# Optimization experiments

Measured on AMD Instinct MI355X. Metric: run time of the kernel, lower is better.

The kernel has to match this reference:

```python
import jax, jax.numpy as jnp
import numpy as np

B, L, C, PS, K, NL, NH, DFF, MAXLEN = 64, 4096, 32, 16, 1024, 4, 8, 2048, 512
D = PS * C          # code_dim = 512
P = L // PS         # num_patches = 256
PA_H = 4            # heads in PatchCrossAttention (largest of {4,2,1} dividing C)
COMMIT = 0.25


def _ln(x, g, b, eps=1e-5):
    m = x.mean(-1, keepdims=True)
    v = x.var(-1, keepdims=True)
    return (x - m) / jnp.sqrt(v + eps) * g + b


def _mha(q, k, v, w_in, b_in, w_out, b_out, nh, mask=None):
    # torch nn.MultiheadAttention math: in_proj weight [3d, d], y = x @ W.T + b
    d = q.shape[-1]
    dh = d // nh
    wq, wk, wv = jnp.split(w_in, 3, axis=0)
    bq, bk, bv = jnp.split(b_in, 3, axis=0)
    qh = (q @ wq.T + bq).reshape(q.shape[0], q.shape[1], nh, dh)
    kh = (k @ wk.T + bk).reshape(k.shape[0], k.shape[1], nh, dh)
    vh = (v @ wv.T + bv).reshape(v.shape[0], v.shape[1], nh, dh)
    scores = jnp.einsum('bqhd,bkhd->bhqk', qh, kh) / jnp.sqrt(jnp.asarray(dh, q.dtype))
    if mask is not None:
        scores = jnp.where(mask, jnp.asarray(-jnp.inf, scores.dtype), scores)
    a = jax.nn.softmax(scores, axis=-1)
    o = jnp.einsum('bhqk,bkhd->bqhd', a, vh).reshape(q.shape[0], q.shape[1], d)
    return o @ w_out.T + b_out


def _forward(x, pa_lq, pa_pos, pa_win, pa_bin, pa_wout, pa_bout,
             pa_ln1g, pa_ln1b, pa_ln2g, pa_ln2b, pa_w1, pa_b1, pa_w2, pa_b2,
             cb, tf_pos, tf_win, tf_bin, tf_wout, tf_bout,
             tf_ln1g, tf_ln1b, tf_ln2g, tf_ln2b,
             tf_w1, tf_b1, tf_w2, tf_b2, fin_g, fin_b):
    Bx = x.shape[0]
    # --- patchify: [B, L, C] -> [B*P, PS, C] ---
    xp = x.reshape(Bx * P, PS, C)
    # --- PatchCrossAttention ---
    x_pos = xp + pa_pos                       # pos emb over patch steps
    lq = jnp.broadcast_to(pa_lq, xp.shape)    # learnable query tokens
    attn = _mha(lq, x_pos, x_pos, pa_win, pa_bin, pa_wout, pa_bout, PA_H)
    xn = _ln(lq + attn, pa_ln1g, pa_ln1b)
    f = jax.nn.gelu(xn @ pa_w1 + pa_b1, approximate=False) @ pa_w2 + pa_b2
    xo = _ln(xn + f, pa_ln2g, pa_ln2b)
    enc = xp + xo                             # residual to raw patch
    # --- flatten + VQ ---
    z = enc.reshape(Bx * P, D)
    d2 = (z * z).sum(1, keepdims=True) + (cb * cb).sum(1) - 2.0 * (z @ cb.T)
    idx = jnp.argmin(d2, axis=1)
    q = cb[idx]
    sg = jax.lax.stop_gradient
    e_loss = jnp.mean((sg(q) - z) ** 2)
    q_loss = jnp.mean((q - sg(z)) ** 2)
    vq_loss = q_loss + COMMIT * e_loss
    quant = z + sg(q - z)                     # straight-through
    # --- causal transformer over code sequence [B, P, D] ---
    t = quant.reshape(Bx, P, D) + tf_pos[:P]
    causal = jnp.triu(jnp.ones((P, P), dtype=bool), 1)
    for i in range(NL):  # post-LN TransformerEncoderLayer, gelu
        a = _mha(t, t, t, tf_win[i], tf_bin[i], tf_wout[i], tf_bout[i], NH, causal)
        t = _ln(t + a, tf_ln1g[i], tf_ln1b[i])
        f = jax.nn.gelu(t @ tf_w1[i] + tf_b1[i], approximate=False) @ tf_w2[i] + tf_b2[i]
        t = _ln(t + f, tf_ln2g[i], tf_ln2b[i])
    y = _ln(t, fin_g, fin_b)
    return y, vq_loss, idx


def setup_inputs() -> dict:
    key = jax.random.key(0)
    ks = iter(jax.random.split(key, 32))
    n = lambda shape, s=0.02: jax.random.normal(next(ks), shape, dtype=jnp.float32) * s
    inp = {
        'x': jax.random.normal(next(ks), (B, L, C), dtype=jnp.float32),
        'pa_lq': n((PS, C)), 'pa_pos': n((PS, C)),
        'pa_win': n((3 * C, C)), 'pa_bin': jnp.zeros((3 * C,), jnp.float32),
        'pa_wout': n((C, C)), 'pa_bout': jnp.zeros((C,), jnp.float32),
        'pa_ln1g': jnp.ones((C,), jnp.float32), 'pa_ln1b': jnp.zeros((C,), jnp.float32),
        'pa_ln2g': jnp.ones((C,), jnp.float32), 'pa_ln2b': jnp.zeros((C,), jnp.float32),
        'pa_w1': n((C, 2 * C)), 'pa_b1': jnp.zeros((2 * C,), jnp.float32),
        'pa_w2': n((2 * C, C)), 'pa_b2': jnp.zeros((C,), jnp.float32),
        'cb': jax.random.uniform(next(ks), (K, D), jnp.float32, -1.0 / K, 1.0 / K),
        'tf_pos': n((MAXLEN, D)),
        'tf_win': n((NL, 3 * D, D)), 'tf_bin': jnp.zeros((NL, 3 * D), jnp.float32),
        'tf_wout': n((NL, D, D)), 'tf_bout': jnp.zeros((NL, D), jnp.float32),
        'tf_ln1g': jnp.ones((NL, D), jnp.float32), 'tf_ln1b': jnp.zeros((NL, D), jnp.float32),
        'tf_ln2g': jnp.ones((NL, D), jnp.float32), 'tf_ln2b': jnp.zeros((NL, D), jnp.float32),
        'tf_w1': n((NL, D, DFF)), 'tf_b1': jnp.zeros((NL, DFF), jnp.float32),
        'tf_w2': n((NL, DFF, D)), 'tf_b2': jnp.zeros((NL, D), jnp.float32),
        'fin_g': jnp.ones((D,), jnp.float32), 'fin_b': jnp.zeros((D,), jnp.float32),
    }
    return inp


def reference(x, pa_lq, pa_pos, pa_win, pa_bin, pa_wout, pa_bout,
              pa_ln1g, pa_ln1b, pa_ln2g, pa_ln2b, pa_w1, pa_b1, pa_w2, pa_b2,
              cb, tf_pos, tf_win, tf_bin, tf_wout, tf_bout,
              tf_ln1g, tf_ln1b, tf_ln2g, tf_ln2b,
              tf_w1, tf_b1, tf_w2, tf_b2, fin_g, fin_b):
    return _forward(x, pa_lq, pa_pos, pa_win, pa_bin, pa_wout, pa_bout,
                    pa_ln1g, pa_ln1b, pa_ln2g, pa_ln2b, pa_w1, pa_b1, pa_w2, pa_b2,
                    cb, tf_pos, tf_win, tf_bin, tf_wout, tf_bout,
                    tf_ln1g, tf_ln1b, tf_ln2g, tf_ln2b,
                    tf_w1, tf_b1, tf_w2, tf_b2, fin_g, fin_b)
```

## Files before the change

kernel.cpp:

```cpp
#include <hip/hip_runtime.h>


#define SQRT1_2F 0.70710678118654752440f

typedef __attribute__((ext_vector_type(8))) short short8;
typedef __attribute__((ext_vector_type(4))) float f32x4;
typedef __attribute__((ext_vector_type(8))) unsigned short ushort8;
typedef unsigned short ushort;
typedef unsigned long long u64;

__device__ __forceinline__ float gelu_exact(float v) {
  return 0.5f * v * (1.0f + erff(v * SQRT1_2F));
}

__device__ __forceinline__ ushort f2b_rne(float f) {
  unsigned u = __float_as_uint(f);
  unsigned r = (u + 0x7fffu + ((u >> 16) & 1u)) >> 16;
  return (ushort)r;
}

__device__ __forceinline__ float b2f(ushort u) {
  return __uint_as_float(((unsigned)u) << 16);
}

__device__ __forceinline__ void gload16(const void* g, void* l) {
  __builtin_amdgcn_global_load_lds(
      (const __attribute__((address_space(1))) void*)g,
      (__attribute__((address_space(3))) void*)l, 16, 0, 0);
}

__device__ __forceinline__ unsigned fkey(float d) {
  unsigned u = __float_as_uint(d);
  return (u & 0x80000000u) ? ~u : (u | 0x80000000u);
}

__global__ __launch_bounds__(64) void patch_setup_kernel(
    const float* __restrict__ lq, const float* __restrict__ win,
    const float* __restrict__ bin, const float* __restrict__ w1,
    const float* __restrict__ w2, float* __restrict__ q16,
    float* __restrict__ w1T, float* __restrict__ w2T) {
  const int tid = threadIdx.x;
#pragma unroll
  for (int q = 0; q < 8; q++) {
    int e = tid + (q << 6);
    int i = e >> 5, c = e & 31;
    const float* wr = win + (size_t)c * 32;
    float acc = bin[c];
#pragma unroll
    for (int d = 0; d < 32; d++) acc += lq[(i << 5) + d] * wr[d];
    q16[e] = acc;
  }
#pragma unroll
  for (int q = 0; q < 32; q++) {
    int e = tid + (q << 6);
    int u = e >> 5, d = e & 31;
    w1T[e] = w1[(size_t)d * 64 + u];
  }
#pragma unroll
  for (int q = 0; q < 32; q++) {
    int e = tid + (q << 6);
    int c = e >> 6, u = e & 63;
    w2T[e] = w2[(size_t)u * 32 + c];
  }
}

__device__ __forceinline__ void ln_16xS(float* buf, const float* g,
                                        const float* bb, int tid) {
  int row = tid >> 2, sub = tid & 3;
  int c0 = sub << 3;
  float* r = buf + row * 34 + c0;
  float v[8];
  float s = 0.f, s2 = 0.f;
#pragma unroll
  for (int n = 0; n < 8; n++) {
    float t = r[n];
    v[n] = t; s += t; s2 += t * t;
  }
  s += __shfl_xor(s, 1);  s += __shfl_xor(s, 2);
  s2 += __shfl_xor(s2, 1); s2 += __shfl_xor(s2, 2);
  float m = s * (1.0f / 32.0f);
  float var = s2 * (1.0f / 32.0f) - m * m;
  float inv = 1.0f / sqrtf(var + 1e-5f);
#pragma unroll
  for (int n = 0; n < 8; n++)
    r[n] = (v[n] - m) * inv * g[c0 + n] + bb[c0 + n];
}

__global__ __launch_bounds__(256) void pkA_kernel(
    const float* __restrict__ x, const float* __restrict__ pos,
    const float* __restrict__ win, const float* __restrict__ bin,
    const float* __restrict__ q16, float* __restrict__ so) {
  __shared__ float sxp[2048];
  __shared__ float skv[4096];
  __shared__ float sq16[16 * 33];
  const int blk = blockIdx.x, t = threadIdx.x;
  const int p0 = blk << 2;
  const int cfix = t & 31;

#pragma unroll
  for (int q = 0; q < 8; q++) {
    int e = t + (q << 8);
    int pl = e >> 9, r = e & 511;
    sxp[e] = x[(size_t)(p0 + pl) * 512 + r] + pos[r];
  }
  if (t < 128) {
#pragma unroll
    for (int q = 0; q < 4; q++) {
      int e = t + (q << 7);
      sq16[(e >> 5) * 33 + (e & 31)] = q16[e];
    }
  }

  float wr0[32], wr1[32];
#pragma unroll
  for (int d4 = 0; d4 < 8; d4++) {
    *(float4*)(wr0 + 4 * d4) =
        *(const float4*)(win + (size_t)(32 + cfix) * 32 + 4 * d4);
    *(float4*)(wr1 + 4 * d4) =
        *(const float4*)(win + (size_t)(64 + cfix) * 32 + 4 * d4);
  }
  const float bk = bin[32 + cfix];
  const float bv = bin[64 + cfix];
  __syncthreads();

#pragma unroll
  for (int q = 0; q < 16; q++) {
    int e = t + (q << 8);
    int pl = e >> 10, rr = e & 1023;
    int w = rr >> 9, rj = rr & 511, j = rj >> 5;
    const float* sx = sxp + (pl << 9) + (j << 5);
    const float* wreg = w ? wr1 : wr0;
    float acc = w ? bv : bk;
#pragma unroll
    for (int d = 0; d < 32; d++) acc += sx[d] * wreg[d];
    skv[e] = acc;
  }
  __syncthreads();

  const int pl = t >> 6, hh = (t >> 4) & 3, i = t & 15;
  const int p = p0 + pl;
  const float* kp = skv + (pl << 10);
  const int hd = hh << 3;

  float sc[16];
#pragma unroll
  for (int j = 0; j < 16; j++) {
    float acc = 0.f;
#pragma unroll
    for (int d = 0; d < 8; d++)
      acc += sq16[i * 33 + hd + d] * kp[(j << 5) + hd + d];
    sc[j] = acc * 0.35355339059327373f;
  }
  {
    float mx = sc[0];
#pragma unroll
    for (int j = 1; j < 16; j++) mx = fmaxf(mx, sc[j]);
    float sm = 0.f;
    float ev[16];
#pragma unroll
    for (int j = 0; j < 16; j++) { ev[j] = expf(sc[j] - mx); sm += ev[j]; }
    float inv = 1.0f / sm;
#pragma unroll
    for (int j = 0; j < 16; j++) sc[j] = ev[j] * inv;
  }
  float* orow = so + (size_t)p * 512 + (i << 5) + hd;
#pragma unroll
  for (int c8 = 0; c8 < 8; c8++) {
    const int c = hd + c8;
    float acc = 0.f;
#pragma unroll
    for (int j = 0; j < 16; j++) acc += sc[j] * kp[512 + (j << 5) + c];
    orow[c8] = acc;
  }
}

__global__ __launch_bounds__(64) void pkB_kernel(
    const float* __restrict__ so_g, const float* __restrict__ x,
    const float* __restrict__ wout, const float* __restrict__ bout,
    const float* __restrict__ lq,
    const float* __restrict__ ln1g, const float* __restrict__ ln1b,
    const float* __restrict__ w1T, const float* __restrict__ b1,
    const float* __restrict__ w2T, const float* __restrict__ b2,
    const float* __restrict__ ln2g, const float* __restrict__ ln2b,
    float* __restrict__ z, ushort* __restrict__ zh,
    ushort* __restrict__ zl, float* __restrict__ znorm) {
  __shared__ float sso[544], sst[544], ssh[1056];
  const int p = blockIdx.x, t = threadIdx.x;
  const int cfix = t & 31;

#pragma unroll
  for (int q = 0; q < 8; q++) {
    int e = t + (q << 6);
    sso[(e >> 5) * 34 + (e & 31)] = so_g[(size_t)p * 512 + e];
  }

  float wo[32];
#pragma unroll
  for (int d4 = 0; d4 < 8; d4++)
    *(float4*)(wo + 4 * d4) = *(const float4*)(wout + (size_t)cfix * 32 + 4 * d4);
  __syncthreads();

#pragma unroll
  for (int q = 0; q < 8; q++) {
    int e = t + (q << 6);
    int i = e >> 5;
    float acc = bout[cfix];
#pragma unroll
    for (int d = 0; d < 32; d++) acc += sso[i * 34 + d] * wo[d];
    sst[i * 34 + cfix] = acc + lq[(i << 5) + cfix];
  }
  __syncthreads();
  ln_16xS(sst, ln1g, ln1b, t);

  float w1r[32];
#pragma unroll
  for (int d4 = 0; d4 < 8; d4++)
    *(float4*)(w1r + 4 * d4) = *(const float4*)(w1T + (size_t)t * 32 + 4 * d4);
  __syncthreads();

#pragma unroll
  for (int q = 0; q < 16; q++) {
    int i = q;
    float acc = b1[t];
#pragma unroll
    for (int d = 0; d < 32; d++) acc += sst[i * 34 + d] * w1r[d];
    ssh[i * 66 + t] = gelu_exact(acc);
  }

  float w2r[64];
#pragma unroll
  for (int u4 = 0; u4 < 16; u4++)
    *(float4*)(w2r + 4 * u4) = *(const float4*)(w2T + (size_t)cfix * 64 + 4 * u4);
  __syncthreads();

#pragma unroll
  for (int q = 0; q < 8; q++) {
    int e = t + (q << 6);
    int i = e >> 5;
    float acc = b2[cfix];
#pragma unroll
    for (int u = 0; u < 64; u++) acc += ssh[i * 66 + u] * w2r[u];
    sso[i * 34 + cfix] = acc + sst[i * 34 + cfix];
  }
  __syncthreads();
  ln_16xS(sso, ln2g, ln2b, t);
  __syncthreads();

  const float* xp = x + (size_t)p * 512;
  const int row = t >> 2, c0v = (t & 3) << 3;
  float zv[8];
#pragma unroll
  for (int n = 0; n < 8; n++)
    zv[n] = xp[(t << 3) + n] + sso[row * 34 + c0v + n];
  float* zo = z + (size_t)p * 512 + (t << 3);
  *(float4*)(zo)     = *(float4*)(zv);
  *(float4*)(zo + 4) = *(float4*)(zv + 4);
  ushort8 hv, lv;
  float s2 = 0.f;
#pragma unroll
  for (int n = 0; n < 8; n++) {
    s2 += zv[n] * zv[n];
    ushort h = f2b_rne(zv[n]);
    hv[n] = h;
    lv[n] = f2b_rne(zv[n] - b2f(h));
  }
  *(ushort8*)(zh + (size_t)p * 512 + (t << 3)) = hv;
  *(ushort8*)(zl + (size_t)p * 512 + (t << 3)) = lv;
#pragma unroll
  for (int off = 1; off < 64; off <<= 1) s2 += __shfl_xor(s2, off);
  if (t == 0) znorm[p] = s2;
}

__global__ __launch_bounds__(64) void cbnorm_kernel(
    const float* __restrict__ cb, float* __restrict__ cbn,
    ushort* __restrict__ ch, ushort* __restrict__ cl) {
  int c = blockIdx.x, lane = threadIdx.x;
  const float* r = cb + (size_t)c * 512 + lane * 8;
  float v[8];
  *(float4*)(v)     = *(const float4*)(r);
  *(float4*)(v + 4) = *(const float4*)(r + 4);
  float s = 0.f;
  ushort8 hv, lv;
#pragma unroll
  for (int n = 0; n < 8; n++) {
    s += v[n] * v[n];
    ushort h = f2b_rne(v[n]);
    hv[n] = h;
    lv[n] = f2b_rne(v[n] - b2f(h));
  }
  *(ushort8*)(ch + (size_t)c * 512 + lane * 8) = hv;
  *(ushort8*)(cl + (size_t)c * 512 + lane * 8) = lv;
#pragma unroll
  for (int off = 1; off < 64; off <<= 1) s += __shfl_xor(s, off);
  if (lane == 0) cbn[c] = s;
}

__global__ __launch_bounds__(256) void gemm_vq_b3(
    const ushort* __restrict__ Ah, const ushort* __restrict__ Al,
    const ushort* __restrict__ Bh, const ushort* __restrict__ Bl,
    const float* __restrict__ znorm, const float* __restrict__ cbn,
    u64* __restrict__ packed) {
  __shared__ ushort sAh[4096], sAl[4096], sBh[4096], sBl[4096];
  const int cpx = gridDim.x >> 3;
  const int bid = (blockIdx.x & 7) * cpx + (blockIdx.x >> 3);
  const int bx = bid & 7, by = bid >> 3;
  const int m0 = by << 7, n0 = bx << 7;
  const int tid = threadIdx.x;
  const int wid = tid >> 6, lane = tid & 63;
  const int wr = wid >> 1, wc = wid & 1;
  const int l15 = lane & 15, lk = lane >> 4;

  const f32x4 fzero = {0.f, 0.f, 0.f, 0.f};
  f32x4 acc[4][4];
#pragma unroll
  for (int i = 0; i < 4; i++)
#pragma unroll
    for (int j = 0; j < 4; j++) acc[i][j] = fzero;

  for (int k0 = 0; k0 < 512; k0 += 32) {
#pragma unroll
    for (int c = 0; c < 2; c++) {
      const int I = tid + (c << 8);
      const int r = I >> 2, kk = (I & 3) << 3;
      const size_t ga = (size_t)(m0 + r) * 512 + k0 + kk;
      const size_t gb = (size_t)(n0 + r) * 512 + k0 + kk;
      const size_t lo = (size_t)((wid << 6) + (c << 8)) * 8;
      gload16(Ah + ga, sAh + lo);
      gload16(Al + ga, sAl + lo);
      gload16(Bh + gb, sBh + lo);
      gload16(Bl + gb, sBl + lo);
    }
    __syncthreads();

    short8 ah[4], al[4], bh[4], bl[4];
#pragma unroll
    for (int m = 0; m < 4; m++) {
      const int ar = ((wr << 6) + (m << 4) + l15) * 32 + lk * 8;
      ah[m] = *(const short8*)(sAh + ar);
      al[m] = *(const short8*)(sAl + ar);
      const int br = ((wc << 6) + (m << 4) + l15) * 32 + lk * 8;
      bh[m] = *(const short8*)(sBh + br);
      bl[m] = *(const short8*)(sBl + br);
    }
#pragma unroll
    for (int m = 0; m < 4; m++)
#pragma unroll
      for (int n = 0; n < 4; n++) {
        acc[m][n] = __builtin_amdgcn_mfma_f32_16x16x32_bf16(ah[m], bh[n],
                                                            acc[m][n], 0, 0, 0);
        acc[m][n] = __builtin_amdgcn_mfma_f32_16x16x32_bf16(ah[m], bl[n],
                                                            acc[m][n], 0, 0, 0);
        acc[m][n] = __builtin_amdgcn_mfma_f32_16x16x32_bf16(al[m], bh[n],
                                                            acc[m][n], 0, 0, 0);
      }
    __syncthreads();
  }

  float zn[4][4];
#pragma unroll
  for (int m = 0; m < 4; m++)
#pragma unroll
    for (int r = 0; r < 4; r++)
      zn[m][r] = znorm[m0 + (wr << 6) + (m << 4) + (lk << 2) + r];
  float cbnv[4];
#pragma unroll
  for (int n = 0; n < 4; n++)
    cbnv[n] = cbn[n0 + (wc << 6) + (n << 4) + l15];

#pragma unroll
  for (int m = 0; m < 4; m++) {
#pragma unroll
    for (int r = 0; r < 4; r++) {
      u64 best = ~0ull;
#pragma unroll
      for (int n = 0; n < 4; n++) {
        const int gcol = n0 + (wc << 6) + (n << 4) + l15;
        float d = (zn[m][r] + cbnv[n]) - 2.0f * acc[m][n][r];
        u64 key = ((u64)fkey(d) << 32) | (unsigned)gcol;
        best = best < key ? best : key;
      }
#pragma unroll
      for (int off = 1; off < 16; off <<= 1) {
        u64 o = __shfl_xor(best, off);
        best = best < o ? best : o;
      }
      if (l15 == 0) {
        const int grow = m0 + (wr << 6) + (m << 4) + (lk << 2) + r;
        atomicMin(&packed[grow], best);
      }
    }
  }
}

__global__ __launch_bounds__(256) void vq_slim_kernel(
    const u64* __restrict__ packed, const float* __restrict__ cb,
    const float* __restrict__ z, const float* __restrict__ tf_pos,
    float* __restrict__ t, ushort* __restrict__ th,
    float* __restrict__ idx_out, float* __restrict__ loss_part) {
  __shared__ float spart[4];
  const int wv = threadIdx.x >> 6;
  const int r = (blockIdx.x << 2) + wv;
  const int lane = threadIdx.x & 63;
  const int bi = (int)(unsigned)(packed[r] & 0xFFFFFFFFull);
  const float* zr = z + (size_t)r * 512 + (lane << 3);
  const float* q = cb + (size_t)bi * 512 + (lane << 3);
  const float* pr = tf_pos + (size_t)(r & 255) * 512 + (lane << 3);
  float zv[8], qv[8], pv[8];
  *(float4*)(zv)     = *(const float4*)(zr);
  *(float4*)(zv + 4) = *(const float4*)(zr + 4);
  *(float4*)(qv)     = *(const float4*)(q);
  *(float4*)(qv + 4) = *(const float4*)(q + 4);
  *(float4*)(pv)     = *(const float4*)(pr);
  *(float4*)(pv + 4) = *(const float4*)(pr + 4);
  float lsum = 0.f;
  float tv[8];
  ushort8 w;
#pragma unroll
  for (int n = 0; n < 8; n++) {
    float diff = qv[n] - zv[n];
    lsum += diff * diff;
    tv[n] = qv[n] + pv[n];
    w[n] = f2b_rne(tv[n]);
  }
  float* to = t + (size_t)r * 512 + (lane << 3);
  *(float4*)(to)     = *(float4*)(tv);
  *(float4*)(to + 4) = *(float4*)(tv + 4);
  *(ushort8*)(th + (size_t)r * 512 + (lane << 3)) = w;
#pragma unroll
  for (int off = 1; off < 64; off <<= 1) lsum += __shfl_xor(lsum, off);
  if (lane == 0) {
    idx_out[r] = (float)bi;
    spart[wv] = lsum;
  }
  __syncthreads();
  if (threadIdx.x == 0)
    loss_part[blockIdx.x] = (spart[0] + spart[1]) + (spart[2] + spart[3]);
}

__global__ __launch_bounds__(256) void loss_reduce_kernel(
    const float* __restrict__ loss_part, float* __restrict__ loss_out) {
  __shared__ float sw[4];
  float s = 0.f;
  for (int i = threadIdx.x; i < 4096; i += 256) s += loss_part[i];
#pragma unroll
  for (int off = 1; off < 64; off <<= 1) s += __shfl_xor(s, off);
  const int wv = threadIdx.x >> 6;
  if ((threadIdx.x & 63) == 0) sw[wv] = s;
  __syncthreads();
  if (threadIdx.x == 0)
    loss_out[0] = ((sw[0] + sw[1]) + (sw[2] + sw[3])) * (1.25f / 8388608.0f);
}

template <int OUTMODE>
__global__ __launch_bounds__(256) void gemm_bf16_kernel(
    const ushort* __restrict__ A, const ushort* __restrict__ B,
    const float* __restrict__ bias, void* __restrict__ Cout,
    int M, int N, int K) {
  __shared__ ushort As[4096];
  __shared__ ushort Bs[4096];
  const int nbx = N >> 7;
  const int cpx = gridDim.x >> 3;
  const int bid = (blockIdx.x & 7) * cpx + (blockIdx.x >> 3);
  const int bx = bid % nbx, by = bid / nbx;
  const int m0 = by << 7, n0 = bx << 7;
  const int tid = threadIdx.x;
  const int wid = tid >> 6, lane = tid & 63;
  const int wr = wid >> 1, wc = wid & 1;
  const int l15 = lane & 15, lk = lane >> 4;

  const f32x4 fzero = {0.f, 0.f, 0.f, 0.f};
  f32x4 acc[4][4];
#pragma unroll
  for (int i = 0; i < 4; i++)
#pragma unroll
    for (int j = 0; j < 4; j++) acc[i][j] = fzero;

  for (int k0 = 0; k0 < K; k0 += 32) {
#pragma unroll
    for (int c = 0; c < 2; c++) {
      const int I = tid + (c << 8);
      const int r = I >> 2, kk = (I & 3) << 3;
      gload16(A + (size_t)(m0 + r) * K + k0 + kk,
              As + (size_t)((wid << 6) + (c << 8)) * 8);
      gload16(B + (size_t)(n0 + r) * K + k0 + kk,
              Bs + (size_t)((wid << 6) + (c << 8)) * 8);
    }
    __syncthreads();

    short8 a[4], b[4];
#pragma unroll
    for (int m = 0; m < 4; m++) {
      const int ar = (wr << 6) + (m << 4) + l15;
      a[m] = *(const short8*)(As + ar * 32 + lk * 8);
      const int br = (wc << 6) + (m << 4) + l15;
      b[m] = *(const short8*)(Bs + br * 32 + lk * 8);
    }
#pragma unroll
    for (int m = 0; m < 4; m++)
#pragma unroll
      for (int n = 0; n < 4; n++)
        acc[m][n] = __builtin_amdgcn_mfma_f32_16x16x32_bf16(a[m], b[n],
                                                            acc[m][n], 0, 0, 0);
    __syncthreads();
  }

  float bv[4];
#pragma unroll
  for (int n = 0; n < 4; n++)
    bv[n] = bias[n0 + (wc << 6) + (n << 4) + l15];

#pragma unroll
  for (int m = 0; m < 4; m++) {
#pragma unroll
    for (int n = 0; n < 4; n++) {
      const int gcol = n0 + (wc << 6) + (n << 4) + l15;
#pragma unroll
      for (int r = 0; r < 4; r++) {
        const int grow = m0 + (wr << 6) + (m << 4) + (lk << 2) + r;
        float v = acc[m][n][r] + bv[n];
        if (OUTMODE == 0) {
          ((float*)Cout)[(size_t)grow * N + gcol] = v;
        } else if (OUTMODE == 1) {
          ((ushort*)Cout)[(size_t)grow * N + gcol] = f2b_rne(gelu_exact(v));
        } else {
          ((ushort*)Cout)[(size_t)grow * N + gcol] = f2b_rne(v);
        }
      }
    }
  }
}

__global__ void cvt_flat(const float* __restrict__ in, ushort* __restrict__ out,
                         int n) {
  int i = blockIdx.x * blockDim.x + threadIdx.x;
  const int stride = gridDim.x * blockDim.x;
  for (; i < n; i += stride) out[i] = f2b_rne(in[i]);
}

__global__ __launch_bounds__(256) void cvt_tr(const float* __restrict__ in,
                                              ushort* __restrict__ out,
                                              int R, int C) {
  __shared__ float tile[32][33];
  const int bc = blockIdx.x, br = blockIdx.y, lay = blockIdx.z;
  const float* src = in + (size_t)lay * R * C;
  ushort* dst = out + (size_t)lay * R * C;
  const int tid = threadIdx.x;
#pragma unroll
  for (int q = 0; q < 4; q++) {
    int idx = tid + (q << 8);
    int rr = idx >> 5, cc = idx & 31;
    tile[rr][cc] = src[(size_t)(br * 32 + rr) * C + bc * 32 + cc];
  }
  __syncthreads();
#pragma unroll
  for (int q = 0; q < 4; q++) {
    int idx = tid + (q << 8);
    int co = idx >> 5, ro = idx & 31;
    dst[(size_t)(bc * 32 + co) * R + br * 32 + ro] = f2b_rne(tile[ro][co]);
  }
}

__global__ __launch_bounds__(64) void attn_mfma_kernel(
    const ushort* __restrict__ qkv, ushort* __restrict__ o) {
  __shared__ ushort lds[8192];
  char* KsB = (char*)lds;
  char* VtB = (char*)(lds + 4096);
  const int bid = blockIdx.x;
  const int xcd = bid & 7, slot = bid >> 3;
  const int b = (xcd << 3) | (slot >> 5);
  const int h = (slot >> 2) & 7;
  const int qb = slot & 3;
  const int lane = threadIdx.x;
  const int l15 = lane & 15, lk4 = lane >> 4;

  short8 qf[4][2];
#pragma unroll
  for (int m = 0; m < 4; m++)
#pragma unroll
    for (int kc = 0; kc < 2; kc++)
      qf[m][kc] = *(const short8*)(qkv +
          (size_t)(b * 256 + qb * 64 + m * 16 + l15) * 1536 +
          h * 64 + kc * 32 + lk4 * 8);

  const f32x4 fz = {0.f, 0.f, 0.f, 0.f};
  f32x4 O[4][4];
#pragma unroll
  for (int m = 0; m < 4; m++)
#pragma unroll
    for (int n = 0; n < 4; n++) O[m][n] = fz;
  float lsum[4][4];
#pragma unroll
  for (int m = 0; m < 4; m++)
#pragma unroll
    for (int r = 0; r < 4; r++) lsum[m][r] = 0.f;

  for (int jt = 0; jt <= qb; jt++) {
    ushort8 kv[8], vv[8];
    const ushort* krow = qkv + (size_t)(b * 256 + jt * 64 + lane) * 1536 +
                         512 + h * 64;
#pragma unroll
    for (int u = 0; u < 8; u++) kv[u] = ((const ushort8*)krow)[u];
#pragma unroll
    for (int u = 0; u < 8; u++) vv[u] = ((const ushort8*)(krow + 512))[u];
    __syncthreads();
    {
      const int rx = (lane & 7) << 4;
#pragma unroll
      for (int u = 0; u < 8; u++)
        *(ushort8*)(KsB + lane * 128 + ((u << 4) ^ rx)) = kv[u];
#pragma unroll
      for (int u = 0; u < 8; u++)
#pragma unroll
        for (int i = 0; i < 8; i++) {
          const int d = u * 8 + i;
          *(ushort*)(VtB + ((d * 128 + lane * 2) ^ ((d & 7) << 4))) =
              (ushort)vv[u][i];
        }
    }
    __syncthreads();

    f32x4 sacc[4][4];
#pragma unroll
    for (int m = 0; m < 4; m++)
#pragma unroll
      for (int n = 0; n < 4; n++) sacc[m][n] = fz;
#pragma unroll
    for (int kc = 0; kc < 2; kc++) {
      short8 bf[4];
#pragma unroll
      for (int n = 0; n < 4; n++) {
        const int row = n * 16 + l15;
        bf[n] = *(const short8*)(KsB + row * 128 +
                                 ((kc * 64 + lk4 * 16) ^ ((row & 7) << 4)));
      }
#pragma unroll
      for (int m = 0; m < 4; m++)
#pragma unroll
        for (int n = 0; n < 4; n++)
          sacc[m][n] = __builtin_amdgcn_mfma_f32_16x16x32_bf16(
              qf[m][kc], bf[n], sacc[m][n], 0, 0, 0);
    }
    __syncthreads();

    const bool diag = (jt == qb);
#pragma unroll
    for (int m = 0; m < 4; m++)
#pragma unroll
      for (int n = 0; n < 4; n++)
#pragma unroll
        for (int r = 0; r < 4; r++) {
          const int ql = m * 16 + lk4 * 4 + r;
          const int jl = n * 16 + l15;
          float e = __expf(sacc[m][n][r] * 0.125f);
          if (diag && jl > ql) e = 0.f;
          const ushort pu = f2b_rne(e);
          lsum[m][r] += b2f(pu);
          *(ushort*)(KsB + ql * 128 + ((jl * 2) ^ ((ql & 7) << 4))) = pu;
        }
    __syncthreads();

#pragma unroll
    for (int kc = 0; kc < 2; kc++) {
      short8 pf[4], vf[4];
#pragma unroll
      for (int m = 0; m < 4; m++) {
        const int row = m * 16 + l15;
        pf[m] = *(const short8*)(KsB + row * 128 +
                                 ((kc * 64 + lk4 * 16) ^ ((row & 7) << 4)));
      }
#pragma unroll
      for (int n = 0; n < 4; n++) {
        const int row = n * 16 + l15;
        vf[n] = *(const short8*)(VtB + row * 128 +
                                 ((kc * 64 + lk4 * 16) ^ ((row & 7) << 4)));
      }
#pragma unroll
      for (int m = 0; m < 4; m++)
#pragma unroll
        for (int n = 0; n < 4; n++)
          O[m][n] = __builtin_amdgcn_mfma_f32_16x16x32_bf16(
              pf[m], vf[n], O[m][n], 0, 0, 0);
    }
  }

  float inv[4][4];
#pragma unroll
  for (int m = 0; m < 4; m++)
#pragma unroll
    for (int r = 0; r < 4; r++) {
      float v = lsum[m][r];
      v += __shfl_xor(v, 1); v += __shfl_xor(v, 2);
      v += __shfl_xor(v, 4); v += __shfl_xor(v, 8);
      inv[m][r] = 1.0f / v;
    }
#pragma unroll
  for (int m = 0; m < 4; m++)
#pragma unroll
    for (int n = 0; n < 4; n++)
#pragma unroll
      for (int r = 0; r < 4; r++) {
        const int row = b * 256 + qb * 64 + m * 16 + lk4 * 4 + r;
        const int col = h * 64 + n * 16 + l15;
        o[(size_t)row * 512 + col] = f2b_rne(O[m][n][r] * inv[m][r]);
      }
}

__global__ __launch_bounds__(256) void ln_kernel(
    const float* __restrict__ xin, const float* __restrict__ addin,
    const float* __restrict__ g, const float* __restrict__ bb,
    float* __restrict__ outp, ushort* __restrict__ outb) {
  const int r = blockIdx.x * 4 + (threadIdx.x >> 6);
  const int lane = threadIdx.x & 63;
  const float* xr = xin + (size_t)r * 512 + lane * 8;
  float v[8];
  *(float4*)(v)     = *(const float4*)(xr);
  *(float4*)(v + 4) = *(const float4*)(xr + 4);
  if (addin) {
    const float* ar = addin + (size_t)r * 512 + lane * 8;
    float w[8];
    *(float4*)(w)     = *(const float4*)(ar);
    *(float4*)(w + 4) = *(const float4*)(ar + 4);
#pragma unroll
    for (int n = 0; n < 8; n++) v[n] += w[n];
  }
  float s = 0.f, s2 = 0.f;
#pragma unroll
  for (int n = 0; n < 8; n++) { s += v[n]; s2 += v[n] * v[n]; }
#pragma unroll
  for (int off = 1; off < 64; off <<= 1) {
    s += __shfl_xor(s, off);
    s2 += __shfl_xor(s2, off);
  }
  float m = s * (1.0f / 512.0f);
  float var = s2 * (1.0f / 512.0f) - m * m;
  float inv = 1.0f / sqrtf(var + 1e-5f);
  const int c0 = lane * 8;
  float outv[8];
#pragma unroll
  for (int n = 0; n < 8; n++) outv[n] = (v[n] - m) * inv * g[c0 + n] + bb[c0 + n];
  float* orow = outp + (size_t)r * 512 + c0;
  *(float4*)(orow)     = *(float4*)(outv);
  *(float4*)(orow + 4) = *(float4*)(outv + 4);
  if (outb) {
    ushort8 w;
#pragma unroll
    for (int n = 0; n < 8; n++) w[n] = f2b_rne(outv[n]);
    *(ushort8*)(outb + (size_t)r * 512 + c0) = w;
  }
}

extern "C" void kernel_launch(void* const* d_in, const int* in_sizes, int n_in,
                              void* d_out, int out_size, void* d_ws, size_t ws_size,
                              hipStream_t stream) {
  const float* x       = (const float*)d_in[0];
  const float* pa_lq   = (const float*)d_in[1];
  const float* pa_pos  = (const float*)d_in[2];
  const float* pa_win  = (const float*)d_in[3];
  const float* pa_bin  = (const float*)d_in[4];
  const float* pa_wout = (const float*)d_in[5];
  const float* pa_bout = (const float*)d_in[6];
  const float* pa_ln1g = (const float*)d_in[7];
  const float* pa_ln1b = (const float*)d_in[8];
  const float* pa_ln2g = (const float*)d_in[9];
  const float* pa_ln2b = (const float*)d_in[10];
  const float* pa_w1   = (const float*)d_in[11];
  const float* pa_b1   = (const float*)d_in[12];
  const float* pa_w2   = (const float*)d_in[13];
  const float* pa_b2   = (const float*)d_in[14];
  const float* cb      = (const float*)d_in[15];
  const float* tf_pos  = (const float*)d_in[16];
  const float* tf_win  = (const float*)d_in[17];
  const float* tf_bin  = (const float*)d_in[18];
  const float* tf_wout = (const float*)d_in[19];
  const float* tf_bout = (const float*)d_in[20];
  const float* tf_ln1g = (const float*)d_in[21];
  const float* tf_ln1b = (const float*)d_in[22];
  const float* tf_ln2g = (const float*)d_in[23];
  const float* tf_ln2b = (const float*)d_in[24];
  const float* tf_w1   = (const float*)d_in[25];
  const float* tf_b1   = (const float*)d_in[26];
  const float* tf_w2   = (const float*)d_in[27];
  const float* tf_b2   = (const float*)d_in[28];
  const float* fin_g   = (const float*)d_in[29];
  const float* fin_b   = (const float*)d_in[30];

  float* yout = (float*)d_out;
  float* loss_out = yout + 8388608;
  float* idx_out = loss_out + 1;

  float* ws   = (float*)d_ws;
  float* z    = ws;
  float* tb   = z + 8388608;
  float* bufA = tb + 8388608;
  float* bufC = bufA + 16777216;
  float* wreg = bufC + 8388608;
  float* treg = wreg + 6291456;
  float* cbn  = treg + 4194304;
  float* q16  = cbn + 1024;
  float* w1T  = q16 + 512;
  float* w2T  = w1T + 2048;
  float* znorm = w2T + 2048;
  u64*   packed = (u64*)(znorm + 16384);
  float* loss_part = (float*)(packed + 16384);

  ushort* win_b  = (ushort*)wreg;
  ushort* wout_b = win_b + 3145728;
  ushort* w1t_b  = wout_b + 1048576;
  ushort* w2t_b  = w1t_b + 4194304;
  ushort* tbh    = (ushort*)treg;
  ushort* qkvh   = (ushort*)bufA;
  ushort* abh    = (ushort*)z;
  ushort* zh_b   = (ushort*)bufC;
  ushort* zl_b   = zh_b + 8388608;
  ushort* ch_b   = (ushort*)treg;
  ushort* cl_b   = ch_b + 524288;

  hipMemsetAsync(packed, 0xFF, 16384 * sizeof(u64), stream);
  cbnorm_kernel<<<1024, 64, 0, stream>>>(cb, cbn, ch_b, cl_b);
  patch_setup_kernel<<<1, 64, 0, stream>>>(pa_lq, pa_win, pa_bin, pa_w1,
                                           pa_w2, q16, w1T, w2T);

  pkA_kernel<<<4096, 256, 0, stream>>>(x, pa_pos, pa_win, pa_bin, q16, bufA);
  pkB_kernel<<<16384, 64, 0, stream>>>(bufA, x, pa_wout, pa_bout, pa_lq,
                                       pa_ln1g, pa_ln1b, w1T, pa_b1,
                                       w2T, pa_b2, pa_ln2g, pa_ln2b, z,
                                       zh_b, zl_b, znorm);

  cvt_flat<<<2048, 256, 0, stream>>>(tf_win, win_b, 3145728);
  cvt_flat<<<1024, 256, 0, stream>>>(tf_wout, wout_b, 1048576);
  cvt_tr<<<dim3(64, 16, 4), 256, 0, stream>>>(tf_w1, w1t_b, 512, 2048);
  cvt_tr<<<dim3(16, 64, 4), 256, 0, stream>>>(tf_w2, w2t_b, 2048, 512);

  gemm_vq_b3<<<dim3(1024), 256, 0, stream>>>(zh_b, zl_b, ch_b, cl_b,
                                             znorm, cbn, packed);
  vq_slim_kernel<<<4096, 256, 0, stream>>>(packed, cb, z, tf_pos, tb, tbh,
                                           idx_out, loss_part);
  loss_reduce_kernel<<<1, 256, 0, stream>>>(loss_part, loss_out);

  for (int l = 0; l < 4; l++) {
    gemm_bf16_kernel<2><<<dim3(128 * 12), 256, 0, stream>>>(
        tbh, win_b + (size_t)l * 1536 * 512, tf_bin + l * 1536, qkvh,
        16384, 1536, 512);
    attn_mfma_kernel<<<dim3(2048), 64, 0, stream>>>(qkvh, abh);
    gemm_bf16_kernel<0><<<dim3(128 * 4), 256, 0, stream>>>(
        abh, wout_b + (size_t)l * 512 * 512, tf_bout + l * 512, bufC,
        16384, 512, 512);
    ln_kernel<<<dim3(4096), 256, 0, stream>>>(tb, bufC, tf_ln1g + l * 512,
                                              tf_ln1b + l * 512, tb, tbh);
    gemm_bf16_kernel<1><<<dim3(128 * 16), 256, 0, stream>>>(
        tbh, w1t_b + (size_t)l * 1048576, tf_b1 + l * 2048, qkvh,
        16384, 2048, 512);
    gemm_bf16_kernel<0><<<dim3(128 * 4), 256, 0, stream>>>(
        qkvh, w2t_b + (size_t)l * 1048576, tf_b2 + l * 512, bufC,
        16384, 512, 2048);
    ln_kernel<<<dim3(4096), 256, 0, stream>>>(tb, bufC, tf_ln2g + l * 512,
                                              tf_ln2b + l * 512, tb, tbh);
  }
  ln_kernel<<<dim3(4096), 256, 0, stream>>>(tb, nullptr, fin_g, fin_b, yout,
                                            nullptr);

  (void)in_sizes; (void)n_in; (void)out_size; (void)ws_size;
}
```

Before: 1.409 ms.

## Widen patch kernel to 256 threads and emit bf16 projection outputs

pkB_kernel now runs with 256 threads per patch instead of 64, spreading the per-patch matmul loops across more lanes and leaving LayerNorm and the output stage to the first wave. The transformer out-projection and FFN2 GEMMs now use the bf16-output GEMM variant, and ln_kernel reads the residual addend as bf16. This halves the write and read traffic of the intermediate projections. The cost is bf16 rounding on the residual branch before LayerNorm, plus idle waves during the serial LN stages of pkB.

```diff
diff --git a/kernel.cpp b/kernel.cpp
--- a/kernel.cpp
+++ b/kernel.cpp
@@ -174,7 +174,7 @@
   }
 }
 
-__global__ __launch_bounds__(64) void pkB_kernel(
+__global__ __launch_bounds__(256) void pkB_kernel(
     const float* __restrict__ so_g, const float* __restrict__ x,
     const float* __restrict__ wout, const float* __restrict__ bout,
     const float* __restrict__ lq,
@@ -186,11 +186,11 @@
     ushort* __restrict__ zl, float* __restrict__ znorm) {
   __shared__ float sso[544], sst[544], ssh[1056];
   const int p = blockIdx.x, t = threadIdx.x;
-  const int cfix = t & 31;
-
-#pragma unroll
-  for (int q = 0; q < 8; q++) {
-    int e = t + (q << 6);
+  const int cfix = t & 31, ufix = t & 63;
+
+#pragma unroll
+  for (int q = 0; q < 2; q++) {
+    int e = t + (q << 8);
     sso[(e >> 5) * 34 + (e & 31)] = so_g[(size_t)p * 512 + e];
   }
 
@@ -201,8 +201,8 @@
   __syncthreads();
 
 #pragma unroll
-  for (int q = 0; q < 8; q++) {
-    int e = t + (q << 6);
+  for (int q = 0; q < 2; q++) {
+    int e = t + (q << 8);
     int i = e >> 5;
     float acc = bout[cfix];
 #pragma unroll
@@ -210,21 +210,22 @@
     sst[i * 34 + cfix] = acc + lq[(i << 5) + cfix];
   }
   __syncthreads();
-  ln_16xS(sst, ln1g, ln1b, t);
+  if (t < 64) ln_16xS(sst, ln1g, ln1b, t);
 
   float w1r[32];
 #pragma unroll
   for (int d4 = 0; d4 < 8; d4++)
-    *(float4*)(w1r + 4 * d4) = *(const float4*)(w1T + (size_t)t * 32 + 4 * d4);
-  __syncthreads();
-
-#pragma unroll
-  for (int q = 0; q < 16; q++) {
-    int i = q;
-    float acc = b1[t];
+    *(float4*)(w1r + 4 * d4) = *(const float4*)(w1T + (size_t)ufix * 32 + 4 * d4);
+  __syncthreads();
+
+#pragma unroll
+  for (int q = 0; q < 4; q++) {
+    int e = t + (q << 8);
+    int i = e >> 6;
+    float acc = b1[ufix];
 #pragma unroll
     for (int d = 0; d < 32; d++) acc += sst[i * 34 + d] * w1r[d];
-    ssh[i * 66 + t] = gelu_exact(acc);
+    ssh[i * 66 + ufix] = gelu_exact(acc);
   }
 
   float w2r[64];
@@ -234,8 +235,8 @@
   __syncthreads();
 
 #pragma unroll
-  for (int q = 0; q < 8; q++) {
-    int e = t + (q << 6);
+  for (int q = 0; q < 2; q++) {
+    int e = t + (q << 8);
     int i = e >> 5;
     float acc = b2[cfix];
 #pragma unroll
@@ -243,32 +244,34 @@
     sso[i * 34 + cfix] = acc + sst[i * 34 + cfix];
   }
   __syncthreads();
-  ln_16xS(sso, ln2g, ln2b, t);
-  __syncthreads();
-
-  const float* xp = x + (size_t)p * 512;
-  const int row = t >> 2, c0v = (t & 3) << 3;
-  float zv[8];
-#pragma unroll
-  for (int n = 0; n < 8; n++)
-    zv[n] = xp[(t << 3) + n] + sso[row * 34 + c0v + n];
-  float* zo = z + (size_t)p * 512 + (t << 3);
-  *(float4*)(zo)     = *(float4*)(zv);
-  *(float4*)(zo + 4) = *(float4*)(zv + 4);
-  ushort8 hv, lv;
-  float s2 = 0.f;
-#pragma unroll
-  for (int n = 0; n < 8; n++) {
-    s2 += zv[n] * zv[n];
-    ushort h = f2b_rne(zv[n]);
-    hv[n] = h;
-    lv[n] = f2b_rne(zv[n] - b2f(h));
-  }
-  *(ushort8*)(zh + (size_t)p * 512 + (t << 3)) = hv;
-  *(ushort8*)(zl + (size_t)p * 512 + (t << 3)) = lv;
-#pragma unroll
-  for (int off = 1; off < 64; off <<= 1) s2 += __shfl_xor(s2, off);
-  if (t == 0) znorm[p] = s2;
+  if (t < 64) ln_16xS(sso, ln2g, ln2b, t);
+  __syncthreads();
+
+  if (t < 64) {
+    const float* xp = x + (size_t)p * 512;
+    const int row = t >> 2, c0v = (t & 3) << 3;
+    float zv[8];
+#pragma unroll
+    for (int n = 0; n < 8; n++)
+      zv[n] = xp[(t << 3) + n] + sso[row * 34 + c0v + n];
+    float* zo = z + (size_t)p * 512 + (t << 3);
+    *(float4*)(zo)     = *(float4*)(zv);
+    *(float4*)(zo + 4) = *(float4*)(zv + 4);
+    ushort8 hv, lv;
+    float s2 = 0.f;
+#pragma unroll
+    for (int n = 0; n < 8; n++) {
+      s2 += zv[n] * zv[n];
+      ushort h = f2b_rne(zv[n]);
+      hv[n] = h;
+      lv[n] = f2b_rne(zv[n] - b2f(h));
+    }
+    *(ushort8*)(zh + (size_t)p * 512 + (t << 3)) = hv;
+    *(ushort8*)(zl + (size_t)p * 512 + (t << 3)) = lv;
+#pragma unroll
+    for (int off = 1; off < 64; off <<= 1) s2 += __shfl_xor(s2, off);
+    if (t == 0) znorm[p] = s2;
+  }
 }
 
 __global__ __launch_bounds__(64) void cbnorm_kernel(
@@ -706,7 +709,7 @@
 }
 
 __global__ __launch_bounds__(256) void ln_kernel(
-    const float* __restrict__ xin, const float* __restrict__ addin,
+    const float* __restrict__ xin, const ushort* __restrict__ addin_b,
     const float* __restrict__ g, const float* __restrict__ bb,
     float* __restrict__ outp, ushort* __restrict__ outb) {
   const int r = blockIdx.x * 4 + (threadIdx.x >> 6);
@@ -715,13 +718,10 @@
   float v[8];
   *(float4*)(v)     = *(const float4*)(xr);
   *(float4*)(v + 4) = *(const float4*)(xr + 4);
-  if (addin) {
-    const float* ar = addin + (size_t)r * 512 + lane * 8;
-    float w[8];
-    *(float4*)(w)     = *(const float4*)(ar);
-    *(float4*)(w + 4) = *(const float4*)(ar + 4);
-#pragma unroll
-    for (int n = 0; n < 8; n++) v[n] += w[n];
+  if (addin_b) {
+    ushort8 a = *(const ushort8*)(addin_b + (size_t)r * 512 + lane * 8);
+#pragma unroll
+    for (int n = 0; n < 8; n++) v[n] += b2f(a[n]);
   }
   float s = 0.f, s2 = 0.f;
 #pragma unroll
@@ -812,6 +812,7 @@
   ushort* abh    = (ushort*)z;
   ushort* zh_b   = (ushort*)bufC;
   ushort* zl_b   = zh_b + 8388608;
+  ushort* projh  = (ushort*)bufC;
   ushort* ch_b   = (ushort*)treg;
   ushort* cl_b   = ch_b + 524288;
 
@@ -821,10 +822,10 @@
                                            pa_w2, q16, w1T, w2T);
 
   pkA_kernel<<<4096, 256, 0, stream>>>(x, pa_pos, pa_win, pa_bin, q16, bufA);
-  pkB_kernel<<<16384, 64, 0, stream>>>(bufA, x, pa_wout, pa_bout, pa_lq,
-                                       pa_ln1g, pa_ln1b, w1T, pa_b1,
-                                       w2T, pa_b2, pa_ln2g, pa_ln2b, z,
-                                       zh_b, zl_b, znorm);
+  pkB_kernel<<<16384, 256, 0, stream>>>(bufA, x, pa_wout, pa_bout, pa_lq,
+                                        pa_ln1g, pa_ln1b, w1T, pa_b1,
+                                        w2T, pa_b2, pa_ln2g, pa_ln2b, z,
+                                        zh_b, zl_b, znorm);
 
   cvt_flat<<<2048, 256, 0, stream>>>(tf_win, win_b, 3145728);
   cvt_flat<<<1024, 256, 0, stream>>>(tf_wout, wout_b, 1048576);
@@ -842,18 +843,18 @@
         tbh, win_b + (size_t)l * 1536 * 512, tf_bin + l * 1536, qkvh,
         16384, 1536, 512);
     attn_mfma_kernel<<<dim3(2048), 64, 0, stream>>>(qkvh, abh);
-    gemm_bf16_kernel<0><<<dim3(128 * 4), 256, 0, stream>>>(
-        abh, wout_b + (size_t)l * 512 * 512, tf_bout + l * 512, bufC,
+    gemm_bf16_kernel<2><<<dim3(128 * 4), 256, 0, stream>>>(
+        abh, wout_b + (size_t)l * 512 * 512, tf_bout + l * 512, projh,
         16384, 512, 512);
-    ln_kernel<<<dim3(4096), 256, 0, stream>>>(tb, bufC, tf_ln1g + l * 512,
+    ln_kernel<<<dim3(4096), 256, 0, stream>>>(tb, projh, tf_ln1g + l * 512,
                                               tf_ln1b + l * 512, tb, tbh);
     gemm_bf16_kernel<1><<<dim3(128 * 16), 256, 0, stream>>>(
         tbh, w1t_b + (size_t)l * 1048576, tf_b1 + l * 2048, qkvh,
         16384, 2048, 512);
-    gemm_bf16_kernel<0><<<dim3(128 * 4), 256, 0, stream>>>(
-        qkvh, w2t_b + (size_t)l * 1048576, tf_b2 + l * 512, bufC,
+    gemm_bf16_kernel<2><<<dim3(128 * 4), 256, 0, stream>>>(
+        qkvh, w2t_b + (size_t)l * 1048576, tf_b2 + l * 512, projh,
         16384, 512, 2048);
-    ln_kernel<<<dim3(4096), 256, 0, stream>>>(tb, bufC, tf_ln2g + l * 512,
+    ln_kernel<<<dim3(4096), 256, 0, stream>>>(tb, projh, tf_ln2g + l * 512,
                                               tf_ln2b + l * 512, tb, tbh);
   }
   ln_kernel<<<dim3(4096), 256, 0, stream>>>(tb, nullptr, fin_g, fin_b, yout,
```

After: 1.500 ms. +6.5%, slower.
